# Performance work log

Hardware: AMD Instinct MI355X
Metric: run time of the kernel (lower is better)

The kernel has to match this reference:

```python
import jax, jax.numpy as jnp
import numpy as np

B, L, D = 8, 4096, 4096
E, R, K = 8, 16, 2
ALPHA = 1.0
EPS = 1e-5

def setup_inputs() -> dict:
    key = jax.random.key(0)
    ks = jax.random.split(key, 5)
    x = jax.random.normal(ks[0], (B, L, D), dtype=jnp.float32)
    gate_w = jax.random.normal(ks[1], (E, D), dtype=jnp.float32) * 0.02
    gate_b = jnp.zeros((E,), dtype=jnp.float32)
    A_w = jax.random.normal(ks[2], (E, R, D), dtype=jnp.float32) * 0.02
    B_w = jax.random.normal(ks[3], (E, D, R), dtype=jnp.float32) * 0.02
    gamma = jnp.ones((D,), dtype=jnp.float32)
    beta = jnp.zeros((D,), dtype=jnp.float32)
    return {"x": x, "gate_w": gate_w, "gate_b": gate_b, "A_w": A_w,
            "B_w": B_w, "gamma": gamma, "beta": beta}

def reference(x, gate_w, gate_b, A_w, B_w, gamma, beta):
    scale = ALPHA / R
    # pooled hidden state per sequence: [B, D]
    h = x.mean(axis=1)
    # router: gate logits -> top-k -> softmax over selected
    logits = h @ gate_w.T + gate_b                     # [B, E]
    top_vals, top_idx = jax.lax.top_k(logits, K)       # [B, K]
    w = jax.nn.softmax(top_vals, axis=-1)              # [B, K]
    # gather selected experts' LoRA factors
    A_sel = A_w[top_idx]                               # [B, K, R, D]
    B_sel = B_w[top_idx]                               # [B, K, D, R]
    z = jnp.einsum('bkrd,bd->bkr', A_sel, h)           # down-proj
    eo = jnp.einsum('bkdr,bkr->bkd', B_sel, z) * scale # up-proj
    delta = jnp.sum(w[..., None] * eo, axis=1)         # [B, D]
    # residual + LayerNorm (broadcast delta over seq dim)
    y = x + delta[:, None, :]
    mu = y.mean(axis=-1, keepdims=True)
    var = y.var(axis=-1, keepdims=True)
    return (y - mu) * jax.lax.rsqrt(var + EPS) * gamma + beta
```

## Files before the change

kernel.cpp:

```cpp
#include <hip/hip_runtime.h>

#define BB    8
#define LSEQ  4096
#define DD    4096
#define EE    8
#define RR    16
#define KK    2
#define NSLICE 128
#define LORA_SCALE (1.0f / 16.0f)
#define LN_EPS 1e-5f

typedef float f4 __attribute__((ext_vector_type(4)));

__device__ __forceinline__ float wave_sum(float v) {
#pragma unroll
    for (int off = 32; off > 0; off >>= 1)
        v += __shfl_xor(v, off, 64);
    return v;
}

__device__ __forceinline__ float dot4(f4 a, f4 b) {
    return a.x * b.x + a.y * b.y + a.z * b.z + a.w * b.w;
}

__global__ __launch_bounds__(256) void colsum_kernel(
    const f4* __restrict__ x, f4* __restrict__ partial, int rows_per_slice)
{
    const int tid = threadIdx.x;
    const int bid = blockIdx.x;
    const int b  = bid >> 7;
    const int sl = bid & (NSLICE - 1);
    const size_t row0 = (size_t)b * LSEQ + (size_t)sl * rows_per_slice;
    const f4* p = x + row0 * (DD / 4);

    f4 acc[4];
#pragma unroll
    for (int i = 0; i < 4; ++i) acc[i] = (f4)(0.f);

#pragma unroll 2
    for (int l = 0; l < rows_per_slice; ++l) {
        const f4* pr = p + (size_t)l * (DD / 4);
#pragma unroll
        for (int i = 0; i < 4; ++i)
            acc[i] += __builtin_nontemporal_load(&pr[tid + i * 256]);
    }
    f4* dst = partial + ((size_t)sl * BB + b) * (DD / 4);
#pragma unroll
    for (int i = 0; i < 4; ++i) dst[tid + i * 256] = acc[i];
}

__global__ __launch_bounds__(1024) void router_delta_kernel(
    const f4* __restrict__ partial, int nslice,
    const f4* __restrict__ gate_w, const float* __restrict__ gate_b,
    const f4* __restrict__ A_w, const f4* __restrict__ B_w,
    f4* __restrict__ delta)
{
    __shared__ float redl[EE * 16];
    __shared__ float lgbuf[EE];
    __shared__ float redz[KK * RR * 16];
    __shared__ float zbuf[KK * RR];
    __shared__ int   sel[KK];
    __shared__ float wsel[KK];

    const int b = blockIdx.x;
    const int tid = threadIdx.x;
    const int lane = tid & 63;
    const int wid = tid >> 6;

    f4 acc = (f4)(0.f);
#pragma unroll 8
    for (int sl = 0; sl < nslice; ++sl)
        acc += partial[((size_t)sl * BB + b) * (DD / 4) + tid];
    const f4 h = acc * (1.0f / LSEQ);

#pragma unroll
    for (int e = 0; e < EE; ++e) {
        float s = wave_sum(dot4(h, gate_w[e * (DD / 4) + tid]));
        if (lane == 0) redl[e * 16 + wid] = s;
    }
    __syncthreads();
    if (tid < EE) {
        float s = 0.f;
#pragma unroll
        for (int w = 0; w < 16; ++w) s += redl[tid * 16 + w];
        lgbuf[tid] = s + gate_b[tid];
    }
    __syncthreads();
    if (tid == 0) {
        int i0 = 0;
        for (int e = 1; e < EE; ++e) if (lgbuf[e] > lgbuf[i0]) i0 = e;
        int i1 = (i0 == 0) ? 1 : 0;
        for (int e = 0; e < EE; ++e) if (e != i0 && lgbuf[e] > lgbuf[i1]) i1 = e;
        float e1 = __expf(lgbuf[i1] - lgbuf[i0]);
        float inv = 1.0f / (1.0f + e1);
        sel[0] = i0; sel[1] = i1;
        wsel[0] = inv; wsel[1] = e1 * inv;
    }
    __syncthreads();

    const f4* A0 = A_w + (size_t)sel[0] * RR * (DD / 4);
    const f4* A1 = A_w + (size_t)sel[1] * RR * (DD / 4);
#pragma unroll
    for (int r = 0; r < RR; ++r) {
        float s0 = wave_sum(dot4(h, A0[r * (DD / 4) + tid]));
        float s1 = wave_sum(dot4(h, A1[r * (DD / 4) + tid]));
        if (lane == 0) {
            redz[r * 16 + wid] = s0;
            redz[(RR + r) * 16 + wid] = s1;
        }
    }
    __syncthreads();
    if (tid < KK * RR) {
        float s = 0.f;
#pragma unroll
        for (int w = 0; w < 16; ++w) s += redz[tid * 16 + w];
        zbuf[tid] = s;
    }
    __syncthreads();

    const float w0 = wsel[0], w1 = wsel[1];
    const f4* B0 = B_w + (size_t)sel[0] * DD * (RR / 4);
    const f4* B1 = B_w + (size_t)sel[1] * DD * (RR / 4);
    f4 o;
#pragma unroll
    for (int c = 0; c < 4; ++c) {
        const int d = tid * 4 + c;
        float s0 = 0.f, s1 = 0.f;
#pragma unroll
        for (int rv = 0; rv < RR / 4; ++rv) {
            f4 b0 = B0[d * (RR / 4) + rv];
            f4 b1 = B1[d * (RR / 4) + rv];
            s0 += b0.x * zbuf[rv * 4] + b0.y * zbuf[rv * 4 + 1]
                + b0.z * zbuf[rv * 4 + 2] + b0.w * zbuf[rv * 4 + 3];
            s1 += b1.x * zbuf[RR + rv * 4] + b1.y * zbuf[RR + rv * 4 + 1]
                + b1.z * zbuf[RR + rv * 4 + 2] + b1.w * zbuf[RR + rv * 4 + 3];
        }
        float v = LORA_SCALE * (w0 * s0 + w1 * s1);
        if (c == 0) o.x = v; else if (c == 1) o.y = v; else if (c == 2) o.z = v; else o.w = v;
    }
    delta[(size_t)b * (DD / 4) + tid] = o;
}

__global__ __launch_bounds__(256) void resid_ln_kernel(
    const f4* __restrict__ x, const f4* __restrict__ delta,
    const f4* __restrict__ gamma, const f4* __restrict__ beta,
    f4* __restrict__ out)
{
    const int tid = threadIdx.x;
    const int lane = tid & 63, wid = tid >> 6;
    const int rgroup = gridDim.x - 1 - blockIdx.x;
    const int row = rgroup * 4 + wid;
    const int b = row >> 12;
    const f4* xr = x + (size_t)row * (DD / 4);
    const f4* dr = delta + (size_t)b * (DD / 4);

    f4 v[16];
    float sum = 0.f, sq = 0.f;
#pragma unroll
    for (int i = 0; i < 16; ++i) {
        const int idx = lane + i * 64;
        f4 xv = __builtin_nontemporal_load(&xr[idx]);
        f4 dv = dr[idx];
        xv += dv;
        v[i] = xv;
        sum += xv.x + xv.y + xv.z + xv.w;
        sq  += xv.x * xv.x + xv.y * xv.y + xv.z * xv.z + xv.w * xv.w;
    }
    sum = wave_sum(sum);
    sq  = wave_sum(sq);
    const float mean = sum * (1.0f / DD);
    const float var  = sq * (1.0f / DD) - mean * mean;
    const float rstd = rsqrtf(var + LN_EPS);

    f4* orow = out + (size_t)row * (DD / 4);
#pragma unroll
    for (int i = 0; i < 16; ++i) {
        const int idx = lane + i * 64;
        f4 gv = gamma[idx];
        f4 bv = beta[idx];
        f4 xv = v[i];
        f4 o;
        o.x = (xv.x - mean) * rstd * gv.x + bv.x;
        o.y = (xv.y - mean) * rstd * gv.y + bv.y;
        o.z = (xv.z - mean) * rstd * gv.z + bv.z;
        o.w = (xv.w - mean) * rstd * gv.w + bv.w;
        __builtin_nontemporal_store(o, &orow[idx]);
    }
}

extern "C" void kernel_launch(void* const* d_in, const int* in_sizes, int n_in,
                              void* d_out, int out_size, void* d_ws, size_t ws_size,
                              hipStream_t stream) {
    const float* x      = (const float*)d_in[0];
    const float* gate_w = (const float*)d_in[1];
    const float* gate_b = (const float*)d_in[2];
    const float* A_w    = (const float*)d_in[3];
    const float* B_w    = (const float*)d_in[4];
    const float* gamma  = (const float*)d_in[5];
    const float* beta   = (const float*)d_in[6];
    float* out = (float*)d_out;
    float* ws  = (float*)d_ws;

    float* partial = ws;
    float* delta   = ws + (size_t)NSLICE * BB * DD;

    colsum_kernel<<<BB * NSLICE, 256, 0, stream>>>(
        (const f4*)x, (f4*)partial, LSEQ / NSLICE);

    router_delta_kernel<<<BB, 1024, 0, stream>>>(
        (const f4*)partial, NSLICE, (const f4*)gate_w, gate_b,
        (const f4*)A_w, (const f4*)B_w, (f4*)delta);

    resid_ln_kernel<<<BB * LSEQ / 4, 256, 0, stream>>>(
        (const f4*)x, (const f4*)delta,
        (const f4*)gamma, (const f4*)beta, (f4*)out);
}
```

Before: 353.2 us.

## Fuse colsum, router and residual LayerNorm into one cooperative kernel

Replaces the three separate launches with one cooperative kernel that uses grid-wide syncs between phases: column sums, then the router and LoRA delta computed by 8 blocks, then residual plus LayerNorm. Each block then processes the same 32-row chunk it summed, in reverse row order, hoping to reuse recently loaded x from cache. This removes inter-kernel launch gaps. In exchange, the grid is capped at 1024 resident blocks, which gives less latency hiding in the LayerNorm phase, and it adds grid.sync cost. Most blocks also sit idle during the router phase. It falls back to the old three-kernel path if the cooperative launch fails.

```diff
diff --git a/kernel.cpp b/kernel.cpp
--- a/kernel.cpp
+++ b/kernel.cpp
@@ -1,4 +1,7 @@
 #include <hip/hip_runtime.h>
+#include <hip/hip_cooperative_groups.h>
+
+namespace cg = cooperative_groups;
 
 #define BB    8
 #define LSEQ  4096
@@ -7,6 +10,8 @@
 #define RR    16
 #define KK    2
 #define NSLICE 128
+#define ROWS_PER_CHUNK 32
+#define NBLK (BB * NSLICE)
 #define LORA_SCALE (1.0f / 16.0f)
 #define LN_EPS 1e-5f
 
@@ -21,6 +26,171 @@
 
 __device__ __forceinline__ float dot4(f4 a, f4 b) {
     return a.x * b.x + a.y * b.y + a.z * b.z + a.w * b.w;
+}
+
+__global__ __launch_bounds__(256, 4) void fused_kernel(
+    const f4* __restrict__ x,
+    const f4* __restrict__ gate_w, const float* __restrict__ gate_b,
+    const f4* __restrict__ A_w, const f4* __restrict__ B_w,
+    const f4* __restrict__ gamma, const f4* __restrict__ beta,
+    f4* __restrict__ out, f4* __restrict__ partial, f4* __restrict__ delta)
+{
+    __shared__ float redl[EE * 4];
+    __shared__ float lgbuf[EE];
+    __shared__ float redz[KK * RR * 4];
+    __shared__ float zbuf[KK * RR];
+    __shared__ int   sel[KK];
+    __shared__ float wsel[KK];
+
+    cg::grid_group grid = cg::this_grid();
+    const int tid = threadIdx.x;
+    const int bid = blockIdx.x;
+    const int lane = tid & 63, wid = tid >> 6;
+
+    {
+        const int b  = bid >> 7;
+        const int sl = bid & (NSLICE - 1);
+        const f4* p = x + ((size_t)b * LSEQ + (size_t)sl * ROWS_PER_CHUNK) * (DD / 4);
+        f4 a0 = (f4)(0.f), a1 = (f4)(0.f), a2 = (f4)(0.f), a3 = (f4)(0.f);
+#pragma unroll 4
+        for (int l = 0; l < ROWS_PER_CHUNK; ++l) {
+            const f4* pr = p + (size_t)l * (DD / 4);
+            a0 += __builtin_nontemporal_load(&pr[tid]);
+            a1 += __builtin_nontemporal_load(&pr[tid + 256]);
+            a2 += __builtin_nontemporal_load(&pr[tid + 512]);
+            a3 += __builtin_nontemporal_load(&pr[tid + 768]);
+        }
+        f4* dst = partial + ((size_t)sl * BB + b) * (DD / 4);
+        dst[tid] = a0; dst[tid + 256] = a1; dst[tid + 512] = a2; dst[tid + 768] = a3;
+    }
+    grid.sync();
+
+    if (bid < BB) {
+        const int b = bid;
+        f4 h[4];
+#pragma unroll
+        for (int i = 0; i < 4; ++i) h[i] = (f4)(0.f);
+#pragma unroll 8
+        for (int sl = 0; sl < NSLICE; ++sl) {
+            const f4* ps = partial + ((size_t)sl * BB + b) * (DD / 4);
+#pragma unroll
+            for (int i = 0; i < 4; ++i) h[i] += ps[tid + i * 256];
+        }
+#pragma unroll
+        for (int i = 0; i < 4; ++i) h[i] *= (1.0f / LSEQ);
+
+#pragma unroll
+        for (int e = 0; e < EE; ++e) {
+            float d = 0.f;
+#pragma unroll
+            for (int i = 0; i < 4; ++i) d += dot4(h[i], gate_w[e * (DD / 4) + tid + i * 256]);
+            float s = wave_sum(d);
+            if (lane == 0) redl[e * 4 + wid] = s;
+        }
+        __syncthreads();
+        if (tid < EE)
+            lgbuf[tid] = redl[tid * 4] + redl[tid * 4 + 1] + redl[tid * 4 + 2] + redl[tid * 4 + 3] + gate_b[tid];
+        __syncthreads();
+        if (tid == 0) {
+            int i0 = 0;
+            for (int e = 1; e < EE; ++e) if (lgbuf[e] > lgbuf[i0]) i0 = e;
+            int i1 = (i0 == 0) ? 1 : 0;
+            for (int e = 0; e < EE; ++e) if (e != i0 && lgbuf[e] > lgbuf[i1]) i1 = e;
+            float e1 = __expf(lgbuf[i1] - lgbuf[i0]);
+            float inv = 1.0f / (1.0f + e1);
+            sel[0] = i0; sel[1] = i1;
+            wsel[0] = inv; wsel[1] = e1 * inv;
+        }
+        __syncthreads();
+
+        const f4* A0 = A_w + (size_t)sel[0] * RR * (DD / 4);
+        const f4* A1 = A_w + (size_t)sel[1] * RR * (DD / 4);
+#pragma unroll
+        for (int r = 0; r < RR; ++r) {
+            float d0 = 0.f, d1 = 0.f;
+#pragma unroll
+            for (int i = 0; i < 4; ++i) {
+                d0 += dot4(h[i], A0[r * (DD / 4) + tid + i * 256]);
+                d1 += dot4(h[i], A1[r * (DD / 4) + tid + i * 256]);
+            }
+            float s0 = wave_sum(d0), s1 = wave_sum(d1);
+            if (lane == 0) { redz[r * 4 + wid] = s0; redz[(RR + r) * 4 + wid] = s1; }
+        }
+        __syncthreads();
+        if (tid < KK * RR)
+            zbuf[tid] = redz[tid * 4] + redz[tid * 4 + 1] + redz[tid * 4 + 2] + redz[tid * 4 + 3];
+        __syncthreads();
+
+        const float w0 = wsel[0], w1 = wsel[1];
+        const f4* B0 = B_w + (size_t)sel[0] * DD * (RR / 4);
+        const f4* B1 = B_w + (size_t)sel[1] * DD * (RR / 4);
+#pragma unroll
+        for (int i = 0; i < 4; ++i) {
+            const int col = tid + i * 256;
+            f4 o;
+#pragma unroll
+            for (int c = 0; c < 4; ++c) {
+                const int d = col * 4 + c;
+                float s0 = 0.f, s1 = 0.f;
+#pragma unroll
+                for (int rv = 0; rv < RR / 4; ++rv) {
+                    f4 b0 = B0[d * (RR / 4) + rv];
+                    f4 b1 = B1[d * (RR / 4) + rv];
+                    s0 += b0.x * zbuf[rv * 4] + b0.y * zbuf[rv * 4 + 1]
+                        + b0.z * zbuf[rv * 4 + 2] + b0.w * zbuf[rv * 4 + 3];
+                    s1 += b1.x * zbuf[RR + rv * 4] + b1.y * zbuf[RR + rv * 4 + 1]
+                        + b1.z * zbuf[RR + rv * 4 + 2] + b1.w * zbuf[RR + rv * 4 + 3];
+                }
+                float val = LORA_SCALE * (w0 * s0 + w1 * s1);
+                if (c == 0) o.x = val; else if (c == 1) o.y = val;
+                else if (c == 2) o.z = val; else o.w = val;
+            }
+            delta[(size_t)b * (DD / 4) + col] = o;
+        }
+    }
+    grid.sync();
+
+    {
+        const int b = bid >> 7;
+        const size_t row_base = (size_t)b * LSEQ + (size_t)(bid & (NSLICE - 1)) * ROWS_PER_CHUNK;
+        const f4* dr = delta + (size_t)b * (DD / 4);
+        for (int rr = 0; rr < 8; ++rr) {
+            const int r = 31 - wid - 4 * rr;
+            const size_t row = row_base + r;
+            const f4* xr = x + row * (DD / 4);
+            f4 v[16];
+            float sum = 0.f, sq = 0.f;
+#pragma unroll
+            for (int i = 0; i < 16; ++i) {
+                const int idx = lane + i * 64;
+                f4 xv = __builtin_nontemporal_load(&xr[idx]);
+                f4 dv = dr[idx];
+                xv += dv;
+                v[i] = xv;
+                sum += xv.x + xv.y + xv.z + xv.w;
+                sq  += xv.x * xv.x + xv.y * xv.y + xv.z * xv.z + xv.w * xv.w;
+            }
+            sum = wave_sum(sum);
+            sq  = wave_sum(sq);
+            const float mean = sum * (1.0f / DD);
+            const float var  = sq * (1.0f / DD) - mean * mean;
+            const float rstd = rsqrtf(var + LN_EPS);
+            f4* orow = out + row * (DD / 4);
+#pragma unroll
+            for (int i = 0; i < 16; ++i) {
+                const int idx = lane + i * 64;
+                f4 gv = gamma[idx];
+                f4 bv = beta[idx];
+                f4 xv = v[i];
+                f4 o;
+                o.x = (xv.x - mean) * rstd * gv.x + bv.x;
+                o.y = (xv.y - mean) * rstd * gv.y + bv.y;
+                o.z = (xv.z - mean) * rstd * gv.z + bv.z;
+                o.w = (xv.w - mean) * rstd * gv.w + bv.w;
+                __builtin_nontemporal_store(o, &orow[idx]);
+            }
+        }
+    }
 }
 
 __global__ __launch_bounds__(256) void colsum_kernel(
@@ -30,13 +200,10 @@
     const int bid = blockIdx.x;
     const int b  = bid >> 7;
     const int sl = bid & (NSLICE - 1);
-    const size_t row0 = (size_t)b * LSEQ + (size_t)sl * rows_per_slice;
-    const f4* p = x + row0 * (DD / 4);
-
+    const f4* p = x + ((size_t)b * LSEQ + (size_t)sl * rows_per_slice) * (DD / 4);
     f4 acc[4];
 #pragma unroll
     for (int i = 0; i < 4; ++i) acc[i] = (f4)(0.f);
-
 #pragma unroll 2
     for (int l = 0; l < rows_per_slice; ++l) {
         const f4* pr = p + (size_t)l * (DD / 4);
@@ -191,27 +358,31 @@
 extern "C" void kernel_launch(void* const* d_in, const int* in_sizes, int n_in,
                               void* d_out, int out_size, void* d_ws, size_t ws_size,
                               hipStream_t stream) {
-    const float* x      = (const float*)d_in[0];
-    const float* gate_w = (const float*)d_in[1];
+    const f4* x       = (const f4*)d_in[0];
+    const f4* gate_w  = (const f4*)d_in[1];
     const float* gate_b = (const float*)d_in[2];
-    const float* A_w    = (const float*)d_in[3];
-    const float* B_w    = (const float*)d_in[4];
-    const float* gamma  = (const float*)d_in[5];
-    const float* beta   = (const float*)d_in[6];
-    float* out = (float*)d_out;
-    float* ws  = (float*)d_ws;
-
-    float* partial = ws;
-    float* delta   = ws + (size_t)NSLICE * BB * DD;
-
-    colsum_kernel<<<BB * NSLICE, 256, 0, stream>>>(
-        (const f4*)x, (f4*)partial, LSEQ / NSLICE);
-
-    router_delta_kernel<<<BB, 1024, 0, stream>>>(
-        (const f4*)partial, NSLICE, (const f4*)gate_w, gate_b,
-        (const f4*)A_w, (const f4*)B_w, (f4*)delta);
-
-    resid_ln_kernel<<<BB * LSEQ / 4, 256, 0, stream>>>(
-        (const f4*)x, (const f4*)delta,
-        (const f4*)gamma, (const f4*)beta, (f4*)out);
-}
+    const f4* A_w     = (const f4*)d_in[3];
+    const f4* B_w     = (const f4*)d_in[4];
+    const f4* gamma   = (const f4*)d_in[5];
+    const f4* beta    = (const f4*)d_in[6];
+    f4* out = (f4*)d_out;
+    float* ws = (float*)d_ws;
+
+    f4* partial = (f4*)ws;
+    f4* delta   = (f4*)(ws + (size_t)NSLICE * BB * DD);
+
+    void* args[] = { (void*)&x, (void*)&gate_w, (void*)&gate_b, (void*)&A_w,
+                     (void*)&B_w, (void*)&gamma, (void*)&beta, (void*)&out,
+                     (void*)&partial, (void*)&delta };
+    hipError_t err = hipLaunchCooperativeKernel(
+        reinterpret_cast<const void*>(&fused_kernel),
+        dim3(NBLK), dim3(256), args, 0, stream);
+
+    if (err != hipSuccess) {
+        colsum_kernel<<<BB * NSLICE, 256, 0, stream>>>(x, partial, LSEQ / NSLICE);
+        router_delta_kernel<<<BB, 1024, 0, stream>>>(
+            partial, NSLICE, gate_w, gate_b, A_w, B_w, delta);
+        resid_ln_kernel<<<BB * LSEQ / 4, 256, 0, stream>>>(
+            x, delta, gamma, beta, out);
+    }
+}
```

Result: slower. 815.0 us (+130.8%).
